# Kernel optimization log

Measured on AMD Instinct MI355X. Metric: run time of the kernel, lower is better.

The kernel has to match this reference:

```python
import jax, jax.numpy as jnp
import numpy as np

B, H, W, C = 2, 128, 128, 96
L = H * W
NUM_HEADS = 6
D_STATE = 16
DT_RANK = 6  # ceil(96/16)
D_CONV = 4
MLP_HIDDEN = 4 * C


def _layernorm(x, g, b, eps=1e-5):
    m = x.mean(-1, keepdims=True)
    v = x.var(-1, keepdims=True)
    return (x - m) * jax.lax.rsqrt(v + eps) * g + b


def _dwconv2d(x, w, b):
    # x: [B,C,H,W], w: [C,1,3,3] depthwise, padding=1 (torch 'same' for k=3)
    y = jax.lax.conv_general_dilated(x, w, (1, 1), [(1, 1), (1, 1)],
                                     dimension_numbers=('NCHW', 'OIHW', 'NCHW'),
                                     feature_group_count=x.shape[1])
    return y + b[None, :, None, None]


def _dwconv1d(x, w):
    # x: [B,C,L], w: [C,1,4]; torch padding='same' for even k=4 pads (1,2); bias is None (conv_bias//2 == 0)
    return jax.lax.conv_general_dilated(x, w, (1,), [(1, 2)],
                                        dimension_numbers=('NCH', 'OIH', 'NCH'),
                                        feature_group_count=x.shape[1])


def _rope(x):
    # x: [b, H, W, c]; 2D axial rotary embedding, k_max = c//4 per axis
    b, h, w, c = x.shape
    k_max = c // 4
    theta = 1.0 / (10000.0 ** (jnp.arange(k_max, dtype=jnp.float32) / k_max))
    ang_h = jnp.broadcast_to(jnp.arange(h, dtype=jnp.float32)[:, None, None] * theta, (h, w, k_max))
    ang_w = jnp.broadcast_to(jnp.arange(w, dtype=jnp.float32)[None, :, None] * theta, (h, w, k_max))
    angles = jnp.concatenate([ang_h, ang_w], -1)  # [h,w,c//2]
    cos, sin = jnp.cos(angles), jnp.sin(angles)
    xr, xi = x[..., 0::2], x[..., 1::2]  # consecutive pairs -> complex
    out_r = xr * cos - xi * sin
    out_i = xr * sin + xi * cos
    return jnp.stack([out_r, out_i], -1).reshape(x.shape)


def _linear_attention(x, qk_w, qk_b, lepe_w, lepe_b):
    # x: [b, n, c]
    b, n, c = x.shape
    hd = c // NUM_HEADS
    qk = x @ qk_w + qk_b  # [b,n,2c]
    q = jax.nn.elu(qk[..., :c]) + 1.0
    k = jax.nn.elu(qk[..., c:]) + 1.0
    v = x
    q_r = _rope(q.reshape(b, H, W, c)).reshape(b, n, NUM_HEADS, hd).transpose(0, 2, 1, 3)
    k_r = _rope(k.reshape(b, H, W, c)).reshape(b, n, NUM_HEADS, hd).transpose(0, 2, 1, 3)
    qh = q.reshape(b, n, NUM_HEADS, hd).transpose(0, 2, 1, 3)
    kh = k.reshape(b, n, NUM_HEADS, hd).transpose(0, 2, 1, 3)
    vh = v.reshape(b, n, NUM_HEADS, hd).transpose(0, 2, 1, 3)
    kmean = kh.mean(axis=2, keepdims=True)  # [b,h,1,hd]
    zden = 1.0 / (jnp.einsum('bhnd,bhmd->bhnm', qh, kmean) + 1e-6)  # [b,h,n,1]
    scale = n ** (-0.5)
    kv = jnp.einsum('bhnd,bhne->bhde', k_r * scale, vh * scale)  # [b,h,hd,hd]
    out = jnp.einsum('bhnd,bhde->bhne', q_r, kv) * zden
    out = out.transpose(0, 2, 1, 3).reshape(b, n, c)
    v2d = v.reshape(b, H, W, c).transpose(0, 3, 1, 2)
    lepe = _dwconv2d(v2d, lepe_w, lepe_b).transpose(0, 2, 3, 1).reshape(b, n, c)
    return out + lepe


def _selective_scan(u, delta, A, Bm, Cm, Dv):
    # u, delta: [b,d,l]; A: [d,n]; Bm, Cm: [b,n,l]; Dv: [d]
    dA = jnp.exp(jnp.einsum('bdl,dn->lbdn', delta, A))
    dBu = jnp.einsum('bdl,bnl,bdl->lbdn', delta, Bm, u)
    Ct = jnp.moveaxis(Cm, -1, 0)  # [l,b,n]

    def step(hcar, inp):
        dA_t, dBu_t, C_t = inp
        hcar = dA_t * hcar + dBu_t  # [b,d,n]
        y_t = jnp.einsum('bdn,bn->bd', hcar, C_t)
        return hcar, y_t

    h0 = jnp.zeros(dA.shape[1:], dtype=u.dtype)
    _, ys = jax.lax.scan(step, h0, (dA, dBu, Ct))  # ys: [l,b,d]
    y = jnp.moveaxis(ys, 0, -1)  # [b,d,l]
    return y + Dv[None, :, None] * u


def setup_inputs() -> dict:
    key = jax.random.key(0)
    ks = iter(jax.random.split(key, 40))

    def rn(shape, s=0.02):
        return jax.random.normal(next(ks), shape, jnp.float32) * s

    dt = jnp.exp(jax.random.uniform(next(ks), (C,), jnp.float32)
                 * (np.log(0.1) - np.log(0.001)) + np.log(0.001))
    dt_proj_b = dt + jnp.log(-jnp.expm1(-dt))
    return {
        'hidden_states': jax.random.normal(next(ks), (B, L, C), jnp.float32),
        'norm_in_g': jnp.ones((C,), jnp.float32),
        'norm_in_b': jnp.zeros((C,), jnp.float32),
        'in_proj_w': rn((C, 3 * C)),
        'dw_w': rn((C, 1, 3, 3)),
        'dw_b': rn((C,)),
        'qk_w': rn((C, 2 * C)),
        'qk_b': rn((2 * C,)),
        'lepe_w': rn((C, 1, 3, 3)),
        'lepe_b': rn((C,)),
        'conv_x_w': rn((C, 1, D_CONV)),
        'conv_z_w': rn((C, 1, D_CONV)),
        'x_proj_w': rn((C, DT_RANK + 2 * D_STATE)),
        'dt_proj_w': rn((DT_RANK, C), DT_RANK ** -0.5),
        'dt_proj_b': dt_proj_b,
        'A_log': jnp.log(jnp.broadcast_to(jnp.arange(1, D_STATE + 1, dtype=jnp.float32), (C, D_STATE)) + 0.0),
        'D': jnp.ones((C,), jnp.float32),
        'out_proj_w': rn((2 * C, C)),
        'proj_out_w': rn((C, C)),
        'proj_out_b': rn((C,)),
        'out_w': rn((2 * C, C)),
        'out_b': rn((C,)),
        'norm_mlp_g': jnp.ones((C,), jnp.float32),
        'norm_mlp_b': jnp.zeros((C,), jnp.float32),
        'fc1_w': rn((C, MLP_HIDDEN)),
        'fc1_b': rn((MLP_HIDDEN,)),
        'fc2_w': rn((MLP_HIDDEN, C)),
        'fc2_b': rn((C,)),
    }


def reference(hidden_states, norm_in_g, norm_in_b, in_proj_w, dw_w, dw_b, qk_w, qk_b,
              lepe_w, lepe_b, conv_x_w, conv_z_w, x_proj_w, dt_proj_w, dt_proj_b,
              A_log, D, out_proj_w, proj_out_w, proj_out_b, out_w, out_b,
              norm_mlp_g, norm_mlp_b, fc1_w, fc1_b, fc2_w, fc2_b):
    b, l, c = hidden_states.shape
    shortcut = hidden_states
    hs = _layernorm(hidden_states, norm_in_g, norm_in_b)
    xzw = jnp.transpose(hs @ in_proj_w, (0, 2, 1))  # [b,3c,l]
    x, z, w_ = jnp.split(xzw, 3, axis=1)  # each [b,c,l]
    # linear-attention branch
    lin_x = jax.nn.silu(_dwconv2d(w_.reshape(b, c, H, W), dw_w, dw_b))
    lin_x = jnp.transpose(lin_x, (0, 2, 3, 1)).reshape(b, l, c)
    lin_x = _linear_attention(lin_x, qk_w, qk_b, lepe_w, lepe_b)
    # selective-scan branch
    A = -jnp.exp(A_log)
    x = jax.nn.silu(_dwconv1d(x, conv_x_w))
    z = jax.nn.silu(_dwconv1d(z, conv_z_w))
    x_dbl = jnp.einsum('bdl,de->ble', x, x_proj_w)
    dt = x_dbl[..., :DT_RANK]
    Bm = jnp.transpose(x_dbl[..., DT_RANK:DT_RANK + D_STATE], (0, 2, 1))
    Cm = jnp.transpose(x_dbl[..., DT_RANK + D_STATE:], (0, 2, 1))
    delta = jax.nn.softplus(jnp.einsum('blr,rd->bdl', dt, dt_proj_w) + dt_proj_b[None, :, None])
    y = _selective_scan(x, delta, A, Bm, Cm, D)
    y = jnp.concatenate([y, z], axis=1)  # [b,2c,l]
    out1 = jnp.transpose(y, (0, 2, 1)) @ out_proj_w  # [b,l,c]
    z_t = jnp.transpose(z, (0, 2, 1))
    out2 = (lin_x * z_t) @ proj_out_w + proj_out_b
    out = jnp.concatenate([out1, out2], -1) @ out_w + out_b
    out = shortcut + out
    h2 = _layernorm(out, norm_mlp_g, norm_mlp_b)
    h2 = jax.nn.gelu(h2 @ fc1_w + fc1_b, approximate=False)
    return out + (h2 @ fc2_w + fc2_b)
```

## Files before the change

### kernel.cpp

```cpp
#include <hip/hip_runtime.h>
#include <hip/hip_bf16.h>
#include <hip/hip_fp16.h>
#include <math.h>

#define B_ 2
#define H_ 128
#define W_ 128
#define C_ 96
#define L_ (H_*W_)
#define BL_ (B_*L_)
#define NH_ 6
#define NPROJ_ 38
#define MLPH_ 384
#define NCH_ 512
#define CHL_ (L_/NCH_)
#define NG_ 32

typedef __attribute__((ext_vector_type(8))) short bf16x8;
typedef __attribute__((ext_vector_type(4))) float f32x4;
typedef __attribute__((ext_vector_type(4))) unsigned short us4v;

#define MFMA16(a,b,c) __builtin_amdgcn_mfma_f32_16x16x32_bf16(a,b,c,0,0,0)

#define WOFF1 0
#define WOFF2 54
#define WOFF3 90
#define WOFF4 126
#define WOFF5 144
#define WOFF6 180
#define WOFF7 252
#define WOFF8 324
#define WFRAGS 333

__device__ __forceinline__ float siluf(float x){ return x / (1.f + __expf(-x)); }
__device__ __forceinline__ unsigned short f2bf(float x){
    __hip_bfloat16 h = __float2bfloat16(x);
    return *reinterpret_cast<unsigned short*>(&h);
}
__device__ __forceinline__ unsigned pack2(float a, float b){
    return (unsigned)f2bf(a) | ((unsigned)f2bf(b) << 16);
}
__device__ __forceinline__ float bf2f(unsigned short u){
    return __uint_as_float((unsigned)u << 16);
}
__device__ __forceinline__ unsigned short f2h(float x){
    __half h = __float2half(x);
    return *reinterpret_cast<unsigned short*>(&h);
}
__device__ __forceinline__ float h2f(unsigned short u){
    __half h = *reinterpret_cast<__half*>(&u);
    return __half2float(h);
}
__device__ __forceinline__ float gelu_fast(float x){
    float u_ = 0.7978845608f*x*(1.f + 0.044715f*x*x);
    float au = fabsf(u_);
    float e = __expf(-2.f*au);
    float th = (1.f - e)/(1.f + e);
    th = copysignf(th, u_);
    return 0.5f*x*(1.f + th);
}

__global__ __launch_bounds__(64) void k_setup(const float* __restrict__ w1,
    const float* __restrict__ w2, const float* __restrict__ w3,
    const float* __restrict__ w4, const float* __restrict__ w5,
    const float* __restrict__ w6, const float* __restrict__ w7,
    const float* __restrict__ dww, const float* __restrict__ lw,
    const float* __restrict__ xpw, const float* __restrict__ cxw,
    const float* __restrict__ czw,
    unsigned short* __restrict__ dst, float2* __restrict__ ctab,
    float* __restrict__ wt9, float* __restrict__ lw9, float* __restrict__ kvacc,
    float* __restrict__ wxT, float* __restrict__ wzT)
{
    int m = blockIdx.y;
    int l = threadIdx.x;
    if (m < 7){
        const float* srcs[7] = {w1,w2,w3,w4,w5,w6,w7};
        const int Ks[7]   = {96,96,192,96,192,96,384};
        const int Ns[7]   = {288,192,96,96,96,384,96};
        const int offs[7] = {WOFF1,WOFF2,WOFF3,WOFF4,WOFF5,WOFF6,WOFF7};
        int f = blockIdx.x;
        int nnt = Ns[m] >> 4, nkf = Ks[m] >> 5;
        if (f >= nnt*nkf) return;
        int kf = f / nnt, nt = f - kf*nnt;
        const float* s = srcs[m];
        unsigned short* d = dst + ((size_t)(offs[m] + f)*64 + l)*8;
        int krow = kf*32 + (l>>4)*8;
        int col  = nt*16 + (l&15);
        #pragma unroll
        for (int j=0;j<8;j++) d[j] = f2bf(s[(size_t)(krow+j)*Ns[m] + col]);
    } else {
        int x = blockIdx.x;
        if (x == 0){
            for (int i=l; i<128*24; i+=64){
                int pos = i/24, p = i%24;
                float th = powf(10000.f, -(float)p/24.f);
                float sn, cs; sincosf((float)pos*th, &sn, &cs);
                ctab[i] = make_float2(cs, sn);
            }
        } else if (x == 1){
            for (int i=l; i<3264; i+=64) kvacc[i] = 0.f;
        } else if (x == 2){
            for (int i=l; i<864; i+=64){
                int c = i/9, tap = i%9;
                wt9[tap*96 + c] = dww[i];
                lw9[tap*96 + c] = lw[i];
            }
        } else if (x == 3){
            for (int f=0; f<9; f++){
                int kf=f/3, nt=f%3;
                unsigned short* d = dst + ((size_t)(WOFF8 + f)*64 + l)*8;
                int krow = kf*32 + (l>>4)*8;
                int col  = nt*16 + (l&15);
                #pragma unroll
                for (int j=0;j<8;j++){
                    float v = (col < NPROJ_) ? xpw[(size_t)(krow+j)*NPROJ_ + col] : 0.f;
                    d[j] = f2bf(v);
                }
            }
        } else if (x == 4){
            for (int i=l; i<384; i+=64){
                int j = i/96, c = i%96;
                wxT[i] = cxw[c*4 + j];
                wzT[i] = czw[c*4 + j];
            }
        }
    }
}

__global__ __launch_bounds__(256) void k_ln_inproj_m(const float* __restrict__ hs,
    const float* __restrict__ gg, const float* __restrict__ bb,
    const unsigned short* __restrict__ wbf,
    unsigned short* __restrict__ xx, unsigned short* __restrict__ zz,
    unsigned short* __restrict__ ww, unsigned short* __restrict__ hsb)
{
    __shared__ unsigned short A[64*128];
    int t = threadIdx.x;
    size_t row0 = (size_t)blockIdx.x * 64;
    {
        int r = t >> 2, q = t & 3;
        const float* src = hs + (row0 + r)*C_ + q*24;
        float v[24];
        float s=0.f, s2=0.f;
        #pragma unroll
        for (int i=0;i<24;i++){ float x=src[i]; v[i]=x; s+=x; s2+=x*x; }
        unsigned short* hdst = hsb + (row0 + r)*C_ + q*24;
        #pragma unroll
        for (int i=0;i<24;i+=4){
            us4v hv; hv[0]=f2bf(v[i]); hv[1]=f2bf(v[i+1]);
            hv[2]=f2bf(v[i+2]); hv[3]=f2bf(v[i+3]);
            *(us4v*)&hdst[i] = hv;
        }
        s += __shfl_xor(s,1); s2 += __shfl_xor(s2,1);
        s += __shfl_xor(s,2); s2 += __shfl_xor(s2,2);
        float mn = s*(1.f/C_);
        float rs = rsqrtf(s2*(1.f/C_) - mn*mn + 1e-5f);
        int base = r*128, sw = (r&7)<<3;
        #pragma unroll
        for (int i=0;i<24;i+=2){
            int c = q*24 + i;
            float a0 = (v[i]  -mn)*rs*gg[c]   + bb[c];
            float a1 = (v[i+1]-mn)*rs*gg[c+1] + bb[c+1];
            *(unsigned*)&A[base + (c ^ sw)] = pack2(a0,a1);
        }
    }
    __syncthreads();
    int w = t>>6, l = t&63, lr = l&15, lh = l>>4;
    int arow = w*16 + lr;
    int abase = arow*128, asw = (arow&7)<<3;
    bf16x8 af[3];
    #pragma unroll
    for (int kf=0;kf<3;kf++)
        af[kf] = *(const bf16x8*)&A[abase + ((kf*32 + lh*8) ^ asw)];
    #pragma unroll 2
    for (int nt=0; nt<18; nt++){
        f32x4 acc = {0.f,0.f,0.f,0.f};
        #pragma unroll
        for (int kf=0;kf<3;kf++){
            bf16x8 bf_ = *(const bf16x8*)(wbf + ((size_t)((WOFF1 + kf*18 + nt)*64 + l))*8);
            acc = MFMA16(af[kf], bf_, acc);
        }
        unsigned short* base_;
        if (nt < 6) base_ = xx; else if (nt < 12) base_ = zz; else base_ = ww;
        int col = (nt%6)*16 + lr;
        unsigned short* dst = base_ + (row0 + w*16 + lh*4)*C_ + col;
        #pragma unroll
        for (int j=0;j<4;j++) dst[(size_t)j*C_] = f2bf(acc[j]);
    }
}

__global__ __launch_bounds__(384) void k_conv1d_xdbl(const unsigned short* __restrict__ xxb,
    const unsigned short* __restrict__ zzb, const float* __restrict__ wxT,
    const float* __restrict__ wzT, const unsigned short* __restrict__ wbf,
    const float* __restrict__ dtw, const float* __restrict__ dtb,
    const float* __restrict__ A_log,
    unsigned short* __restrict__ xsb, unsigned short* __restrict__ zb,
    unsigned short* __restrict__ dlh, float* __restrict__ BC,
    float* __restrict__ Ap, float* __restrict__ Be)
{
    __shared__ unsigned short A[64*128];
    __shared__ float XD[64][8];
    __shared__ float dtws[6][96];
    __shared__ float sdl[64][96];
    __shared__ float sbc[64][32];
    int t = threadIdx.x;
    size_t row0 = (size_t)blockIdx.x * 64;
    int b = (int)(row0 >> 14);
    int l0 = (int)(row0 & 16383);
    for (int i=t; i<576; i+=384) dtws[i/96][i%96] = dtw[i];
    for (int p=t; p<64*24; p+=384){
        int r = p/24, cq = p - r*24, c = cq*4;
        int l = l0 + r;
        float ax0=0.f,ax1=0.f,ax2=0.f,ax3=0.f;
        float az0=0.f,az1=0.f,az2=0.f,az3=0.f;
        #pragma unroll
        for (int j=0;j<4;j++){
            int lq = l - 1 + j;
            if ((unsigned)lq < (unsigned)L_){
                size_t off = ((size_t)(b<<14) + lq)*C_ + c;
                us4v xv = *(const us4v*)&xxb[off];
                us4v zv = *(const us4v*)&zzb[off];
                float4 wx4 = *(const float4*)&wxT[j*96 + c];
                float4 wz4 = *(const float4*)&wzT[j*96 + c];
                ax0 += bf2f(xv[0])*wx4.x; ax1 += bf2f(xv[1])*wx4.y;
                ax2 += bf2f(xv[2])*wx4.z; ax3 += bf2f(xv[3])*wx4.w;
                az0 += bf2f(zv[0])*wz4.x; az1 += bf2f(zv[1])*wz4.y;
                az2 += bf2f(zv[2])*wz4.z; az3 += bf2f(zv[3])*wz4.w;
            }
        }
        ax0=siluf(ax0); ax1=siluf(ax1); ax2=siluf(ax2); ax3=siluf(ax3);
        az0=siluf(az0); az1=siluf(az1); az2=siluf(az2); az3=siluf(az3);
        us4v xo; xo[0]=f2bf(ax0); xo[1]=f2bf(ax1); xo[2]=f2bf(ax2); xo[3]=f2bf(ax3);
        *(us4v*)&xsb[(row0+r)*C_ + c] = xo;
        us4v zo; zo[0]=f2bf(az0); zo[1]=f2bf(az1); zo[2]=f2bf(az2); zo[3]=f2bf(az3);
        *(us4v*)&zb[(row0+r)*C_ + c] = zo;
        int sw = (r&7)<<3;
        *(us4v*)&A[r*128 + (c ^ sw)] = xo;
    }
    __syncthreads();
    int w=t>>6, l=t&63, lr=l&15, lh=l>>4;
    if (w < 4){
        int arow = w*16+lr, asw=(arow&7)<<3;
        bf16x8 af[3];
        #pragma unroll
        for (int kf=0;kf<3;kf++)
            af[kf] = *(const bf16x8*)&A[arow*128 + ((kf*32 + lh*8) ^ asw)];
        #pragma unroll
        for (int nt=0; nt<3; nt++){
            f32x4 acc={0.f,0.f,0.f,0.f};
            #pragma unroll
            for (int kf=0;kf<3;kf++){
                bf16x8 bfr=*(const bf16x8*)(wbf + ((size_t)((WOFF8 + kf*3 + nt)*64 + l))*8);
                acc = MFMA16(af[kf], bfr, acc);
            }
            int col = nt*16 + lr;
            #pragma unroll
            for (int j=0;j<4;j++){
                int row = w*16 + lh*4 + j;
                if (col < 6) XD[row][col] = acc[j];
                else if (col < NPROJ_){
                    BC[(row0+row)*32 + (col-6)] = acc[j];
                    sbc[row][col-6] = acc[j];
                }
            }
        }
    }
    __syncthreads();
    if (t < 256){
        int r = t>>2, q = t&3;
        float xd0=XD[r][0], xd1=XD[r][1], xd2=XD[r][2];
        float xd3=XD[r][3], xd4=XD[r][4], xd5=XD[r][5];
        #pragma unroll
        for (int g=0; g<6; g++){
            int c = q*24 + g*4;
            float4 acc = *(const float4*)&dtb[c];
            float4 w0 = *(const float4*)&dtws[0][c];
            float4 w1 = *(const float4*)&dtws[1][c];
            float4 w2 = *(const float4*)&dtws[2][c];
            float4 w3 = *(const float4*)&dtws[3][c];
            float4 w4 = *(const float4*)&dtws[4][c];
            float4 w5 = *(const float4*)&dtws[5][c];
            acc.x += xd0*w0.x + xd1*w1.x + xd2*w2.x + xd3*w3.x + xd4*w4.x + xd5*w5.x;
            acc.y += xd0*w0.y + xd1*w1.y + xd2*w2.y + xd3*w3.y + xd4*w4.y + xd5*w5.y;
            acc.z += xd0*w0.z + xd1*w1.z + xd2*w2.z + xd3*w3.z + xd4*w4.z + xd5*w5.z;
            acc.w += xd0*w0.w + xd1*w1.w + xd2*w2.w + xd3*w3.w + xd4*w4.w + xd5*w5.w;
            float4 dl;
            dl.x = (acc.x>20.f)? acc.x : __logf(1.f+__expf(acc.x));
            dl.y = (acc.y>20.f)? acc.y : __logf(1.f+__expf(acc.y));
            dl.z = (acc.z>20.f)? acc.z : __logf(1.f+__expf(acc.z));
            dl.w = (acc.w>20.f)? acc.w : __logf(1.f+__expf(acc.w));
            sdl[r][c]=dl.x; sdl[r][c+1]=dl.y; sdl[r][c+2]=dl.z; sdl[r][c+3]=dl.w;
            us4v dh; dh[0]=f2h(dl.x); dh[1]=f2h(dl.y); dh[2]=f2h(dl.z); dh[3]=f2h(dl.w);
            *(us4v*)&dlh[(row0+r)*C_ + c] = dh;
        }
    }
    __syncthreads();
    {
        int c = t>>2, nq = t&3;
        float4 a4 = *(const float4*)&A_log[c*16 + nq*4];
        float a0=-__expf(a4.x), a1=-__expf(a4.y), a2=-__expf(a4.z), a3=-__expf(a4.w);
        int chbase = b*NCH_ + (l0>>5);
        int csw_c = c;
        #pragma unroll
        for (int chunk=0; chunk<2; chunk++){
            float ap0=1.f,ap1=1.f,ap2=1.f,ap3=1.f;
            float be0=0.f,be1=0.f,be2=0.f,be3=0.f;
            for (int i=0;i<CHL_;i++){
                int row = chunk*CHL_ + i;
                float dl = sdl[row][c];
                float u = bf2f(A[row*128 + (csw_c ^ ((row&7)<<3))]);
                float du = dl*u;
                float4 bc = *(const float4*)&sbc[row][nq*4];
                float e0=__expf(dl*a0), e1=__expf(dl*a1), e2=__expf(dl*a2), e3=__expf(dl*a3);
                ap0*=e0; be0=be0*e0+du*bc.x;
                ap1*=e1; be1=be1*e1+du*bc.y;
                ap2*=e2; be2=be2*e2+du*bc.z;
                ap3*=e3; be3=be3*e3+du*bc.w;
            }
            size_t o = (size_t)(chbase+chunk)*1536 + c*16 + nq*4;
            float4 apv={ap0,ap1,ap2,ap3}, bev={be0,be1,be2,be3};
            *(float4*)&Ap[o] = apv;
            *(float4*)&Be[o] = bev;
        }
    }
}

__global__ __launch_bounds__(256) void k_qk_kv(const unsigned short* __restrict__ wwb,
    const float* __restrict__ wt9, const float* __restrict__ dwb,
    const unsigned short* __restrict__ wbf, const float* __restrict__ qkb,
    const float2* __restrict__ ctab, unsigned short* __restrict__ linb,
    unsigned short* __restrict__ qo, float* __restrict__ kvacc)
{
    __shared__ unsigned short A[64*128];
    __shared__ float KR[64*105];
    __shared__ float kmsum[96];
    int t = threadIdx.x;
    size_t row0 = (size_t)blockIdx.x * 64;
    int b = (int)(row0 >> 14);
    int l0 = (int)(row0 & 16383);
    for (int p = t; p < 64*24; p += 256){
        int r = p/24, cq = p - r*24, c = cq*4;
        int ll = l0 + r;
        int hq = ll>>7, wq = ll&127;
        float a0=0.f,a1=0.f,a2=0.f,a3=0.f;
        #pragma unroll
        for (int kh=0; kh<3; kh++){
            int hh = hq + kh - 1;
            if ((unsigned)hh < 128u){
                int base_row = (b<<14) + (hh<<7);
                #pragma unroll
                for (int kw=0; kw<3; kw++){
                    int wp = wq + kw - 1;
                    if ((unsigned)wp < 128u){
                        us4v v = *(const us4v*)&wwb[(size_t)(base_row + wp)*C_ + c];
                        float4 wt = *(const float4*)&wt9[(kh*3+kw)*96 + c];
                        a0 += bf2f(v[0])*wt.x; a1 += bf2f(v[1])*wt.y;
                        a2 += bf2f(v[2])*wt.z; a3 += bf2f(v[3])*wt.w;
                    }
                }
            }
        }
        float4 bv = *(const float4*)&dwb[c];
        us4v o;
        o[0]=f2bf(siluf(a0+bv.x)); o[1]=f2bf(siluf(a1+bv.y));
        o[2]=f2bf(siluf(a2+bv.z)); o[3]=f2bf(siluf(a3+bv.w));
        *(us4v*)&linb[(row0+r)*C_ + c] = o;
        int sw = (r&7)<<3;
        *(us4v*)&A[r*128 + (c ^ sw)] = o;
    }
    if (t < 96) kmsum[t] = 0.f;
    __syncthreads();
    int w=t>>6, l=t&63, lr=l&15, lh=l>>4;
    int arow = w*16+lr; int asw=(arow&7)<<3;
    bf16x8 af[3];
    #pragma unroll
    for (int kf=0;kf<3;kf++)
        af[kf] = *(const bf16x8*)&A[arow*128 + ((kf*32 + lh*8) ^ asw)];
    #pragma unroll 2
    for (int nt=0; nt<12; nt++){
        f32x4 acc={0.f,0.f,0.f,0.f};
        #pragma unroll
        for (int kf=0;kf<3;kf++){
            bf16x8 bfr=*(const bf16x8*)(wbf + ((size_t)((WOFF2 + kf*12 + nt)*64 + l))*8);
            acc = MFMA16(af[kf], bfr, acc);
        }
        int colg = nt*16 + lr;
        float bias = qkb[colg];
        float vv[4];
        #pragma unroll
        for (int j=0;j<4;j++){
            float v = acc[j] + bias;
            vv[j] = (v>0.f)? v+1.f : __expf(v);
        }
        if (nt < 6){
            unsigned short* dp = qo + (row0 + w*16 + lh*4)*C_ + colg;
            #pragma unroll
            for (int j=0;j<4;j++) dp[(size_t)j*C_] = f2bf(vv[j]);
        } else {
            int ck = colg - 96;
            atomicAdd(&kmsum[ck], vv[0]+vv[1]+vv[2]+vv[3]);
            float pv[4];
            #pragma unroll
            for (int j=0;j<4;j++) pv[j] = __shfl_xor(vv[j], 1);
            int p = ck >> 1;
            #pragma unroll
            for (int j=0;j<4;j++){
                int rl = l0 + w*16 + lh*4 + j;
                int hp = rl>>7, wp = rl&127;
                float2 cssn = (p<24)? ctab[hp*24+p] : ctab[wp*24+(p-24)];
                float kr = (ck&1)? (pv[j]*cssn.y + vv[j]*cssn.x)
                                 : (vv[j]*cssn.x - pv[j]*cssn.y);
                KR[(w*16+lh*4+j)*105 + ck] = kr;
            }
        }
    }
    __syncthreads();
    for (int h = w; h < 6; h += 4){
        f32x4 acc = {0.f,0.f,0.f,0.f};
        #pragma unroll
        for (int kk=0; kk<2; kk++){
            union { bf16x8 v; unsigned short u[8]; } afu, bfu;
            #pragma unroll
            for (int j=0;j<8;j++){
                int rr = kk*32 + lh*8 + j;
                afu.u[j] = f2bf(KR[rr*105 + h*16 + lr]);
                bfu.u[j] = A[rr*128 + ((h*16+lr) ^ ((rr&7)<<3))];
            }
            acc = MFMA16(afu.v, bfu.v, acc);
        }
        #pragma unroll
        for (int i=0;i<4;i++)
            atomicAdd(&kvacc[b*1536 + h*256 + (lh*4+i)*16 + lr], acc[i]);
    }
    if (t < 96) atomicAdd(&kvacc[3072 + b*96 + t], kmsum[t]);
}

__global__ __launch_bounds__(384) void k_attnout(const unsigned short* __restrict__ qb,
    const unsigned short* __restrict__ vb, const unsigned short* __restrict__ zb,
    const float* __restrict__ kvacc, const float2* __restrict__ ctab,
    const float* __restrict__ lw9, const float* __restrict__ lb,
    unsigned short* __restrict__ azb)
{
    __shared__ float kvs[1536];
    __shared__ float kms[96];
    int t = threadIdx.x;
    size_t row0 = (size_t)blockIdx.x * 16;
    int b = (int)(row0 >> 14);
    const float invL = 1.f/16384.f;
    for (int i=t; i<1536; i+=384) kvs[i] = kvacc[b*1536+i]*invL;
    if (t < 96) kms[t] = kvacc[3072+b*96+t]*invL;
    __syncthreads();
    int r = t/24, c4 = t%24;
    int c = c4*4;
    int lrow = (int)(row0 & 16383) + r;
    int hp = lrow>>7, wp = lrow&127;
    size_t row = row0 + r;
    us4v qu = *(const us4v*)&qb[row*C_ + c];
    float q0=bf2f(qu[0]), q1=bf2f(qu[1]), q2=bf2f(qu[2]), q3=bf2f(qu[3]);
    int p0 = c>>1, p1 = p0+1;
    float2 cs0 = (p0<24)? ctab[hp*24+p0] : ctab[wp*24+(p0-24)];
    float2 cs1 = (p1<24)? ctab[hp*24+p1] : ctab[wp*24+(p1-24)];
    float4 qr;
    qr.x = q0*cs0.x - q1*cs0.y;
    qr.y = q0*cs0.y + q1*cs0.x;
    qr.z = q2*cs1.x - q3*cs1.y;
    qr.w = q2*cs1.y + q3*cs1.x;
    int h = c4>>2, j = c4&3;
    int dbase = j*4;
    float zp = q0*kms[h*16+dbase]   + q1*kms[h*16+dbase+1]
             + q2*kms[h*16+dbase+2] + q3*kms[h*16+dbase+3];
    zp += __shfl_xor(zp,1);
    zp += __shfl_xor(zp,2);
    float zd = 1.f/(zp + 1e-6f);
    float4 o = {0.f,0.f,0.f,0.f};
    #pragma unroll
    for (int g=0; g<4; g++){
        float4 qg;
        if (g==0) qg = qr;
        else {
            qg.x=__shfl_xor(qr.x,g); qg.y=__shfl_xor(qr.y,g);
            qg.z=__shfl_xor(qr.z,g); qg.w=__shfl_xor(qr.w,g);
        }
        int db = ((j^g)<<2);
        const float* kp = &kvs[h*256 + db*16 + j*4];
        #pragma unroll
        for (int i=0;i<4;i++){
            float qi = (i==0)?qg.x:(i==1)?qg.y:(i==2)?qg.z:qg.w;
            float4 kv4 = *(const float4*)&kp[i*16];
            o.x += qi*kv4.x; o.y += qi*kv4.y;
            o.z += qi*kv4.z; o.w += qi*kv4.w;
        }
    }
    float4 acc = *(const float4*)&lb[c];
    #pragma unroll
    for (int kh=0; kh<3; kh++){
        int hh = hp + kh - 1;
        if ((unsigned)hh < 128u){
            int base_row = (b<<14) + (hh<<7);
            #pragma unroll
            for (int kw=0; kw<3; kw++){
                int wq = wp + kw - 1;
                if ((unsigned)wq < 128u){
                    us4v v = *(const us4v*)&vb[(size_t)(base_row + wq)*C_ + c];
                    float4 wt = *(const float4*)&lw9[(kh*3+kw)*96 + c];
                    acc.x += bf2f(v[0])*wt.x; acc.y += bf2f(v[1])*wt.y;
                    acc.z += bf2f(v[2])*wt.z; acc.w += bf2f(v[3])*wt.w;
                }
            }
        }
    }
    us4v zu = *(const us4v*)&zb[row*C_ + c];
    us4v res;
    res[0] = f2bf((o.x*zd + acc.x)*bf2f(zu[0]));
    res[1] = f2bf((o.y*zd + acc.y)*bf2f(zu[1]));
    res[2] = f2bf((o.z*zd + acc.z)*bf2f(zu[2]));
    res[3] = f2bf((o.w*zd + acc.w)*bf2f(zu[3]));
    *(us4v*)&azb[row*C_ + c] = res;
}

__global__ __launch_bounds__(384) void k_scan2a(const float* __restrict__ Ap,
    const float* __restrict__ Be, float* __restrict__ GA, float* __restrict__ GB)
{
    int t = threadIdx.x; int blk = blockIdx.x;
    int b = blk>>5, g = blk&(NG_-1);
    int idx = (t>>2)*16 + (t&3)*4;
    float4 A = {1.f,1.f,1.f,1.f}, Bv = {0.f,0.f,0.f,0.f};
    for (int j=0;j<16;j++){
        size_t o = ((size_t)(b*NCH_ + g*16 + j))*1536 + idx;
        float4 a = *(const float4*)&Ap[o];
        float4 bb = *(const float4*)&Be[o];
        Bv.x=a.x*Bv.x+bb.x; Bv.y=a.y*Bv.y+bb.y; Bv.z=a.z*Bv.z+bb.z; Bv.w=a.w*Bv.w+bb.w;
        A.x*=a.x; A.y*=a.y; A.z*=a.z; A.w*=a.w;
    }
    size_t o = (size_t)blk*1536 + idx;
    *(float4*)&GA[o] = A;
    *(float4*)&GB[o] = Bv;
}

__global__ __launch_bounds__(384) void k_scan2bc(const float* __restrict__ Ap,
    const float* __restrict__ Be, const float* __restrict__ GA,
    const float* __restrict__ GB, float* __restrict__ Hin)
{
    int t = threadIdx.x; int blk = blockIdx.x;
    int b = blk>>5, g = blk&(NG_-1);
    int idx = (t>>2)*16 + (t&3)*4;
    float4 h = {0.f,0.f,0.f,0.f};
    for (int gg=0; gg<g; gg++){
        size_t o = ((size_t)(b*NG_+gg))*1536 + idx;
        float4 a = *(const float4*)&GA[o];
        float4 bb = *(const float4*)&GB[o];
        h.x=a.x*h.x+bb.x; h.y=a.y*h.y+bb.y; h.z=a.z*h.z+bb.z; h.w=a.w*h.w+bb.w;
    }
    for (int j=0;j<16;j++){
        size_t o = ((size_t)(b*NCH_ + g*16 + j))*1536 + idx;
        *(float4*)&Hin[o] = h;
        float4 a = *(const float4*)&Ap[o];
        float4 bb = *(const float4*)&Be[o];
        h.x=a.x*h.x+bb.x; h.y=a.y*h.y+bb.y; h.z=a.z*h.z+bb.z; h.w=a.w*h.w+bb.w;
    }
}

__global__ __launch_bounds__(384) void k_scan3(const unsigned short* __restrict__ dlh,
    const unsigned short* __restrict__ xsb, const float* __restrict__ BC,
    const float* __restrict__ A_log, const float* __restrict__ Dv,
    const float* __restrict__ Hin, unsigned short* __restrict__ y)
{
    int t = threadIdx.x; int nq = t&3, c = t>>2;
    int blk = blockIdx.x; int b = blk>>9, ch = blk&(NCH_-1);
    float4 a4 = *(const float4*)&A_log[c*16 + nq*4];
    float a0=-__expf(a4.x), a1=-__expf(a4.y), a2=-__expf(a4.z), a3=-__expf(a4.w);
    float4 h = *(const float4*)&Hin[(size_t)blk*1536 + c*16 + nq*4];
    float Dc = Dv[c];
    size_t base = ((size_t)b<<14) + ch*CHL_;
    for (int i=0;i<CHL_;i++){
        size_t row = base + i;
        float dl = h2f(dlh[row*C_+c]);
        float u  = bf2f(xsb[row*C_+c]);
        float du = dl*u;
        float4 bcB = *(const float4*)&BC[row*32 + nq*4];
        float4 bcC = *(const float4*)&BC[row*32 + 16 + nq*4];
        float e0=__expf(dl*a0), e1=__expf(dl*a1), e2=__expf(dl*a2), e3=__expf(dl*a3);
        h.x=h.x*e0+du*bcB.x; h.y=h.y*e1+du*bcB.y;
        h.z=h.z*e2+du*bcB.z; h.w=h.w*e3+du*bcB.w;
        float yv = h.x*bcC.x + h.y*bcC.y + h.z*bcC.z + h.w*bcC.w;
        yv += __shfl_xor(yv,1);
        yv += __shfl_xor(yv,2);
        if (nq == 0) y[row*C_+c] = f2bf(yv + Dc*u);
    }
}

__global__ __launch_bounds__(512) void k_combine_mlp(const unsigned short* __restrict__ yb,
    const unsigned short* __restrict__ zb, const unsigned short* __restrict__ azb,
    const unsigned short* __restrict__ wbf, const float* __restrict__ pob,
    const float* __restrict__ outb, const unsigned short* __restrict__ hsb,
    const float* __restrict__ gg, const float* __restrict__ bb,
    const float* __restrict__ f1b, const float* __restrict__ f2b,
    float* __restrict__ outr)
{
    __shared__ __attribute__((aligned(16))) char POOL[65536];
    __shared__ float LNS[64][2], LNS2[64][2];
    unsigned short* C2 = (unsigned short*)POOL;
    unsigned short* AT = (unsigned short*)POOL;
    unsigned short* HID= (unsigned short*)(POOL + 16384);
    int t=threadIdx.x;
    size_t row0=(size_t)blockIdx.x*64;
    int w=t>>6, l=t&63, lr=l&15, lh=l>>4;
    int rt=w>>1, hf=w&1;
    int arow=rt*16+lr; int asw=(arow&7)<<3;
    size_t gbase = (row0+arow)*C_;
    bf16x8 af1[6], af2[3];
    #pragma unroll
    for (int kf=0;kf<3;kf++){
        af1[kf]   = *(const bf16x8*)&yb[gbase + kf*32 + lh*8];
        af1[3+kf] = *(const bf16x8*)&zb[gbase + kf*32 + lh*8];
        af2[kf]   = *(const bf16x8*)&azb[gbase + kf*32 + lh*8];
    }
    #pragma unroll
    for (int q=0;q<3;q++){
        int nt = hf*3 + q;
        f32x4 a1={0.f,0.f,0.f,0.f}, a2={0.f,0.f,0.f,0.f};
        #pragma unroll
        for (int kf=0;kf<6;kf++){
            bf16x8 b=*(const bf16x8*)(wbf+((size_t)((WOFF3+kf*6+nt)*64+l))*8);
            a1=MFMA16(af1[kf],b,a1);
        }
        #pragma unroll
        for (int kf=0;kf<3;kf++){
            bf16x8 b=*(const bf16x8*)(wbf+((size_t)((WOFF4+kf*6+nt)*64+l))*8);
            a2=MFMA16(af2[kf],b,a2);
        }
        int col=nt*16+lr;
        float pb=pob[col];
        #pragma unroll
        for (int j=0;j<4;j++){
            int row=rt*16+lh*4+j;
            int sw2=(row&7)<<3;
            C2[row*192 + (col^sw2)] = f2bf(a1[j]);
            C2[row*192 + ((96+col)^sw2)] = f2bf(a2[j]+pb);
        }
    }
    __syncthreads();
    bf16x8 af3[6];
    #pragma unroll
    for (int kf=0;kf<6;kf++) af3[kf]=*(const bf16x8*)&C2[arow*192 + ((kf*32+lh*8)^asw)];
    float outv[3][4];
    #pragma unroll
    for (int q=0;q<3;q++){
        int nt = hf*3 + q;
        f32x4 acc={0.f,0.f,0.f,0.f};
        #pragma unroll
        for (int kf=0;kf<6;kf++){
            bf16x8 b=*(const bf16x8*)(wbf+((size_t)((WOFF5+kf*6+nt)*64+l))*8);
            acc=MFMA16(af3[kf],b,acc);
        }
        int col=nt*16+lr;
        float ob=outb[col];
        #pragma unroll
        for (int j=0;j<4;j++){
            size_t row=row0+rt*16+lh*4+j;
            outv[q][j] = acc[j] + ob + bf2f(hsb[row*C_+col]);
        }
    }
    float s_[4], s2_[4];
    #pragma unroll
    for (int j=0;j<4;j++){
        float s=0.f, s2=0.f;
        #pragma unroll
        for (int q=0;q<3;q++){ float v=outv[q][j]; s+=v; s2+=v*v; }
        s_[j]=s; s2_[j]=s2;
    }
    #pragma unroll
    for (int m=1;m<16;m<<=1){
        #pragma unroll
        for (int j=0;j<4;j++){
            s_[j]  += __shfl_xor(s_[j],  m);
            s2_[j] += __shfl_xor(s2_[j], m);
        }
    }
    if (lr==0){
        #pragma unroll
        for (int j=0;j<4;j++){
            int row = rt*16+lh*4+j;
            LNS[row][hf]  = s_[j];
            LNS2[row][hf] = s2_[j];
        }
    }
    __syncthreads();
    #pragma unroll
    for (int j=0;j<4;j++){
        int row = rt*16+lh*4+j;
        float s  = LNS[row][0]  + LNS[row][1];
        float s2 = LNS2[row][0] + LNS2[row][1];
        float mn = s*(1.f/C_);
        float rs = rsqrtf(s2*(1.f/C_) - mn*mn + 1e-5f);
        int sw2 = (row&7)<<3;
        #pragma unroll
        for (int q=0;q<3;q++){
            int col = (hf*3+q)*16+lr;
            AT[row*128 + (col^sw2)] = f2bf((outv[q][j]-mn)*rs*gg[col]+bb[col]);
        }
    }
    __syncthreads();
    {
        bf16x8 af[3];
        #pragma unroll
        for(int kf=0;kf<3;kf++) af[kf]=*(const bf16x8*)&AT[arow*128+((kf*32+lh*8)^asw)];
        #pragma unroll 2
        for(int q=0;q<12;q++){
            int nt = hf*12 + q;
            f32x4 acc={0.f,0.f,0.f,0.f};
            #pragma unroll
            for(int kf=0;kf<3;kf++){
                bf16x8 b=*(const bf16x8*)(wbf+((size_t)((WOFF6+kf*24+nt)*64+l))*8);
                acc=MFMA16(af[kf],b,acc);
            }
            int col=nt*16+lr;
            float bias=f1b[col];
            #pragma unroll
            for(int j=0;j<4;j++){
                int row=rt*16+lh*4+j;
                HID[row*384 + (col^((row&7)<<3))] = f2bf(gelu_fast(acc[j]+bias));
            }
        }
    }
    __syncthreads();
    {
        bf16x8 afh[12];
        #pragma unroll
        for(int kf=0;kf<12;kf++) afh[kf]=*(const bf16x8*)&HID[arow*384+((kf*32+lh*8)^asw)];
        #pragma unroll
        for(int q=0;q<3;q++){
            int nt = hf*3 + q;
            f32x4 acc={0.f,0.f,0.f,0.f};
            #pragma unroll
            for(int kf=0;kf<12;kf++){
                bf16x8 b=*(const bf16x8*)(wbf+((size_t)((WOFF7+kf*6+nt)*64+l))*8);
                acc=MFMA16(afh[kf],b,acc);
            }
            int col=nt*16+lr;
            float bias=f2b[col];
            #pragma unroll
            for(int j=0;j<4;j++){
                size_t row=row0+rt*16+lh*4+j;
                outr[row*C_+col] = outv[q][j] + acc[j] + bias;
            }
        }
    }
}

extern "C" void kernel_launch(void* const* d_in, const int* in_sizes, int n_in,
                              void* d_out, int out_size, void* d_ws, size_t ws_size,
                              hipStream_t stream)
{
    const float* hs        = (const float*)d_in[0];
    const float* norm_in_g = (const float*)d_in[1];
    const float* norm_in_b = (const float*)d_in[2];
    const float* in_proj_w = (const float*)d_in[3];
    const float* dw_w      = (const float*)d_in[4];
    const float* dw_b      = (const float*)d_in[5];
    const float* qk_w      = (const float*)d_in[6];
    const float* qk_b      = (const float*)d_in[7];
    const float* lepe_w    = (const float*)d_in[8];
    const float* lepe_b    = (const float*)d_in[9];
    const float* conv_x_w  = (const float*)d_in[10];
    const float* conv_z_w  = (const float*)d_in[11];
    const float* x_proj_w  = (const float*)d_in[12];
    const float* dt_proj_w = (const float*)d_in[13];
    const float* dt_proj_b = (const float*)d_in[14];
    const float* A_log     = (const float*)d_in[15];
    const float* Dv        = (const float*)d_in[16];
    const float* out_proj_w= (const float*)d_in[17];
    const float* proj_out_w= (const float*)d_in[18];
    const float* proj_out_b= (const float*)d_in[19];
    const float* out_w     = (const float*)d_in[20];
    const float* out_b     = (const float*)d_in[21];
    const float* norm_mlp_g= (const float*)d_in[22];
    const float* norm_mlp_b= (const float*)d_in[23];
    const float* fc1_w     = (const float*)d_in[24];
    const float* fc1_b     = (const float*)d_in[25];
    const float* fc2_w     = (const float*)d_in[26];
    const float* fc2_b     = (const float*)d_in[27];

    float* ws = (float*)d_ws;
    size_t o = 0;
    const size_t USH = (size_t)BL_*C_/2;
    unsigned short* xxb  = (unsigned short*)(ws + o); o += USH;
    unsigned short* zzb  = (unsigned short*)(ws + o); o += USH;
    unsigned short* wwb  = (unsigned short*)(ws + o); o += USH;
    unsigned short* linb = (unsigned short*)(ws + o); o += USH;
    unsigned short* zbuf = (unsigned short*)(ws + o); o += USH;
    unsigned short* xsb  = (unsigned short*)(ws + o); o += USH;
    unsigned short* dlh  = (unsigned short*)(ws + o); o += USH;
    unsigned short* hsb  = (unsigned short*)(ws + o); o += USH;
    float* BC    = ws + o; o += (size_t)BL_*32;
    float* Ap    = ws + o; o += (size_t)B_*NCH_*1536;
    float* Be    = ws + o; o += (size_t)B_*NCH_*1536;
    float* Hin   = ws + o; o += (size_t)B_*NCH_*1536;
    float* GA    = ws + o; o += (size_t)B_*NG_*1536;
    float* GB    = ws + o; o += (size_t)B_*NG_*1536;
    float* kvacc = ws + o; o += 3264;
    float2* ctab = (float2*)(ws + o); o += 6144;
    float* wt9   = ws + o; o += 864;
    float* lw9   = ws + o; o += 864;
    float* wxT   = ws + o; o += 384;
    float* wzT   = ws + o; o += 384;
    unsigned short* wbf = (unsigned short*)(ws + o);

    unsigned short* qb  = xxb;
    unsigned short* yb  = zzb;
    unsigned short* azb = wwb;
    float* outr = (float*)d_out;

    k_setup<<<dim3(72,8), 64, 0, stream>>>(in_proj_w, qk_w, out_proj_w, proj_out_w,
                                           out_w, fc1_w, fc2_w, dw_w, lepe_w,
                                           x_proj_w, conv_x_w, conv_z_w,
                                           wbf, ctab, wt9, lw9, kvacc, wxT, wzT);
    k_ln_inproj_m<<<BL_/64, 256, 0, stream>>>(hs, norm_in_g, norm_in_b, wbf,
                                              xxb, zzb, wwb, hsb);
    k_conv1d_xdbl<<<BL_/64, 384, 0, stream>>>(xxb, zzb, wxT, wzT, wbf,
                                              dt_proj_w, dt_proj_b, A_log,
                                              xsb, zbuf, dlh, BC, Ap, Be);
    k_qk_kv<<<BL_/64, 256, 0, stream>>>(wwb, wt9, dw_b, wbf, qk_b, ctab,
                                        linb, qb, kvacc);
    k_attnout<<<BL_/16, 384, 0, stream>>>(qb, linb, zbuf, kvacc, ctab, lw9, lepe_b, azb);
    k_scan2a<<<B_*NG_, 384, 0, stream>>>(Ap, Be, GA, GB);
    k_scan2bc<<<B_*NG_, 384, 0, stream>>>(Ap, Be, GA, GB, Hin);
    k_scan3<<<B_*NCH_, 384, 0, stream>>>(dlh, xsb, BC, A_log, Dv, Hin, yb);
    k_combine_mlp<<<BL_/64, 512, 0, stream>>>(yb, zbuf, azb, wbf, proj_out_b,
                                              out_b, hsb, norm_mlp_g, norm_mlp_b,
                                              fc1_b, fc2_b, outr);
}
```

Before: 192.2 us.

## Split depthwise conv2d into own kernel and fold chunk-prefix scan into scan3

Moves the 3x3 depthwise conv + SiLU out of k_qk_kv into a standalone elementwise kernel, so k_qk_kv just loads the precomputed activations into shared memory. It also removes the k_scan2bc kernel and the Hin buffer: each k_scan3 block now recomputes its own starting state from the group prefixes (GA/GB) and the preceding chunk summaries within its group. This trades one launch and the Hin write/read for redundant per-block prefix work (up to 31+15 steps) and an extra kernel launch for the conv.

```diff
diff --git a/kernel.cpp b/kernel.cpp
--- a/kernel.cpp
+++ b/kernel.cpp
@@ -186,6 +186,40 @@
         #pragma unroll
         for (int j=0;j<4;j++) dst[(size_t)j*C_] = f2bf(acc[j]);
     }
+}
+
+__global__ __launch_bounds__(256) void k_dwconv2d(const unsigned short* __restrict__ wwb,
+    const float* __restrict__ wt9, const float* __restrict__ dwb,
+    unsigned short* __restrict__ out)
+{
+    int gid = blockIdx.x*256 + threadIdx.x;
+    int row = gid/24, c4 = gid%24; int c = c4*4;
+    int b = row >> 14;
+    int ll = row & (L_-1);
+    int h = ll >> 7, wq = ll & 127;
+    float a0=0.f,a1=0.f,a2=0.f,a3=0.f;
+    #pragma unroll
+    for (int kh=0; kh<3; kh++){
+        int hh = h + kh - 1;
+        if ((unsigned)hh < 128u){
+            int base_row = (b<<14) + (hh<<7);
+            #pragma unroll
+            for (int kw=0; kw<3; kw++){
+                int wp = wq + kw - 1;
+                if ((unsigned)wp < 128u){
+                    us4v v = *(const us4v*)&wwb[(size_t)(base_row + wp)*C_ + c];
+                    float4 wt = *(const float4*)&wt9[(kh*3+kw)*96 + c];
+                    a0 += bf2f(v[0])*wt.x; a1 += bf2f(v[1])*wt.y;
+                    a2 += bf2f(v[2])*wt.z; a3 += bf2f(v[3])*wt.w;
+                }
+            }
+        }
+    }
+    float4 bv = *(const float4*)&dwb[c];
+    us4v o;
+    o[0]=f2bf(siluf(a0+bv.x)); o[1]=f2bf(siluf(a1+bv.y));
+    o[2]=f2bf(siluf(a2+bv.z)); o[3]=f2bf(siluf(a3+bv.w));
+    *(us4v*)&out[(size_t)row*C_ + c] = o;
 }
 
 __global__ __launch_bounds__(384) void k_conv1d_xdbl(const unsigned short* __restrict__ xxb,
@@ -299,7 +333,6 @@
         float4 a4 = *(const float4*)&A_log[c*16 + nq*4];
         float a0=-__expf(a4.x), a1=-__expf(a4.y), a2=-__expf(a4.z), a3=-__expf(a4.w);
         int chbase = b*NCH_ + (l0>>5);
-        int csw_c = c;
         #pragma unroll
         for (int chunk=0; chunk<2; chunk++){
             float ap0=1.f,ap1=1.f,ap2=1.f,ap3=1.f;
@@ -307,7 +340,7 @@
             for (int i=0;i<CHL_;i++){
                 int row = chunk*CHL_ + i;
                 float dl = sdl[row][c];
-                float u = bf2f(A[row*128 + (csw_c ^ ((row&7)<<3))]);
+                float u = bf2f(A[row*128 + (c ^ ((row&7)<<3))]);
                 float du = dl*u;
                 float4 bc = *(const float4*)&sbc[row][nq*4];
                 float e0=__expf(dl*a0), e1=__expf(dl*a1), e2=__expf(dl*a2), e3=__expf(dl*a3);
@@ -324,11 +357,10 @@
     }
 }
 
-__global__ __launch_bounds__(256) void k_qk_kv(const unsigned short* __restrict__ wwb,
-    const float* __restrict__ wt9, const float* __restrict__ dwb,
+__global__ __launch_bounds__(256) void k_qk_kv(const unsigned short* __restrict__ lin,
     const unsigned short* __restrict__ wbf, const float* __restrict__ qkb,
-    const float2* __restrict__ ctab, unsigned short* __restrict__ linb,
-    unsigned short* __restrict__ qo, float* __restrict__ kvacc)
+    const float2* __restrict__ ctab, unsigned short* __restrict__ qo,
+    float* __restrict__ kvacc)
 {
     __shared__ unsigned short A[64*128];
     __shared__ float KR[64*105];
@@ -337,35 +369,10 @@
     size_t row0 = (size_t)blockIdx.x * 64;
     int b = (int)(row0 >> 14);
     int l0 = (int)(row0 & 16383);
-    for (int p = t; p < 64*24; p += 256){
-        int r = p/24, cq = p - r*24, c = cq*4;
-        int ll = l0 + r;
-        int hq = ll>>7, wq = ll&127;
-        float a0=0.f,a1=0.f,a2=0.f,a3=0.f;
-        #pragma unroll
-        for (int kh=0; kh<3; kh++){
-            int hh = hq + kh - 1;
-            if ((unsigned)hh < 128u){
-                int base_row = (b<<14) + (hh<<7);
-                #pragma unroll
-                for (int kw=0; kw<3; kw++){
-                    int wp = wq + kw - 1;
-                    if ((unsigned)wp < 128u){
-                        us4v v = *(const us4v*)&wwb[(size_t)(base_row + wp)*C_ + c];
-                        float4 wt = *(const float4*)&wt9[(kh*3+kw)*96 + c];
-                        a0 += bf2f(v[0])*wt.x; a1 += bf2f(v[1])*wt.y;
-                        a2 += bf2f(v[2])*wt.z; a3 += bf2f(v[3])*wt.w;
-                    }
-                }
-            }
-        }
-        float4 bv = *(const float4*)&dwb[c];
-        us4v o;
-        o[0]=f2bf(siluf(a0+bv.x)); o[1]=f2bf(siluf(a1+bv.y));
-        o[2]=f2bf(siluf(a2+bv.z)); o[3]=f2bf(siluf(a3+bv.w));
-        *(us4v*)&linb[(row0+r)*C_ + c] = o;
+    for (int p = t; p < 64*12; p += 256){
+        int r = p/12, c = (p - r*12)*8;
         int sw = (r&7)<<3;
-        *(us4v*)&A[r*128 + (c ^ sw)] = o;
+        *(uint4*)&A[r*128 + (c ^ sw)] = *(const uint4*)&lin[(row0+r)*C_ + c];
     }
     if (t < 96) kmsum[t] = 0.f;
     __syncthreads();
@@ -536,13 +543,19 @@
     *(float4*)&GB[o] = Bv;
 }
 
-__global__ __launch_bounds__(384) void k_scan2bc(const float* __restrict__ Ap,
-    const float* __restrict__ Be, const float* __restrict__ GA,
-    const float* __restrict__ GB, float* __restrict__ Hin)
-{
-    int t = threadIdx.x; int blk = blockIdx.x;
-    int b = blk>>5, g = blk&(NG_-1);
-    int idx = (t>>2)*16 + (t&3)*4;
+__global__ __launch_bounds__(384) void k_scan3(const unsigned short* __restrict__ dlh,
+    const unsigned short* __restrict__ xsb, const float* __restrict__ BC,
+    const float* __restrict__ A_log, const float* __restrict__ Dv,
+    const float* __restrict__ Ap, const float* __restrict__ Be,
+    const float* __restrict__ GA, const float* __restrict__ GB,
+    unsigned short* __restrict__ y)
+{
+    int t = threadIdx.x; int nq = t&3, c = t>>2;
+    int blk = blockIdx.x; int b = blk>>9, ch = blk&(NCH_-1);
+    int g = ch>>4, j0 = ch&15;
+    int idx = c*16 + nq*4;
+    float4 a4 = *(const float4*)&A_log[idx];
+    float a0=-__expf(a4.x), a1=-__expf(a4.y), a2=-__expf(a4.z), a3=-__expf(a4.w);
     float4 h = {0.f,0.f,0.f,0.f};
     for (int gg=0; gg<g; gg++){
         size_t o = ((size_t)(b*NG_+gg))*1536 + idx;
@@ -550,25 +563,12 @@
         float4 bb = *(const float4*)&GB[o];
         h.x=a.x*h.x+bb.x; h.y=a.y*h.y+bb.y; h.z=a.z*h.z+bb.z; h.w=a.w*h.w+bb.w;
     }
-    for (int j=0;j<16;j++){
-        size_t o = ((size_t)(b*NCH_ + g*16 + j))*1536 + idx;
-        *(float4*)&Hin[o] = h;
+    for (int jj=0; jj<j0; jj++){
+        size_t o = ((size_t)(b*NCH_ + g*16 + jj))*1536 + idx;
         float4 a = *(const float4*)&Ap[o];
         float4 bb = *(const float4*)&Be[o];
         h.x=a.x*h.x+bb.x; h.y=a.y*h.y+bb.y; h.z=a.z*h.z+bb.z; h.w=a.w*h.w+bb.w;
     }
-}
-
-__global__ __launch_bounds__(384) void k_scan3(const unsigned short* __restrict__ dlh,
-    const unsigned short* __restrict__ xsb, const float* __restrict__ BC,
-    const float* __restrict__ A_log, const float* __restrict__ Dv,
-    const float* __restrict__ Hin, unsigned short* __restrict__ y)
-{
-    int t = threadIdx.x; int nq = t&3, c = t>>2;
-    int blk = blockIdx.x; int b = blk>>9, ch = blk&(NCH_-1);
-    float4 a4 = *(const float4*)&A_log[c*16 + nq*4];
-    float a0=-__expf(a4.x), a1=-__expf(a4.y), a2=-__expf(a4.z), a3=-__expf(a4.w);
-    float4 h = *(const float4*)&Hin[(size_t)blk*1536 + c*16 + nq*4];
     float Dc = Dv[c];
     size_t base = ((size_t)b<<14) + ch*CHL_;
     for (int i=0;i<CHL_;i++){
@@ -794,7 +794,6 @@
     float* BC    = ws + o; o += (size_t)BL_*32;
     float* Ap    = ws + o; o += (size_t)B_*NCH_*1536;
     float* Be    = ws + o; o += (size_t)B_*NCH_*1536;
-    float* Hin   = ws + o; o += (size_t)B_*NCH_*1536;
     float* GA    = ws + o; o += (size_t)B_*NG_*1536;
     float* GB    = ws + o; o += (size_t)B_*NG_*1536;
     float* kvacc = ws + o; o += 3264;
@@ -816,15 +815,14 @@
                                            wbf, ctab, wt9, lw9, kvacc, wxT, wzT);
     k_ln_inproj_m<<<BL_/64, 256, 0, stream>>>(hs, norm_in_g, norm_in_b, wbf,
                                               xxb, zzb, wwb, hsb);
+    k_dwconv2d<<<(BL_*24)/256, 256, 0, stream>>>(wwb, wt9, dw_b, linb);
     k_conv1d_xdbl<<<BL_/64, 384, 0, stream>>>(xxb, zzb, wxT, wzT, wbf,
                                               dt_proj_w, dt_proj_b, A_log,
                                               xsb, zbuf, dlh, BC, Ap, Be);
-    k_qk_kv<<<BL_/64, 256, 0, stream>>>(wwb, wt9, dw_b, wbf, qk_b, ctab,
-                                        linb, qb, kvacc);
+    k_qk_kv<<<BL_/64, 256, 0, stream>>>(linb, wbf, qk_b, ctab, qb, kvacc);
     k_attnout<<<BL_/16, 384, 0, stream>>>(qb, linb, zbuf, kvacc, ctab, lw9, lepe_b, azb);
     k_scan2a<<<B_*NG_, 384, 0, stream>>>(Ap, Be, GA, GB);
-    k_scan2bc<<<B_*NG_, 384, 0, stream>>>(Ap, Be, GA, GB, Hin);
-    k_scan3<<<B_*NCH_, 384, 0, stream>>>(dlh, xsb, BC, A_log, Dv, Hin, yb);
+    k_scan3<<<B_*NCH_, 384, 0, stream>>>(dlh, xsb, BC, A_log, Dv, Ap, Be, GA, GB, yb);
     k_combine_mlp<<<BL_/64, 512, 0, stream>>>(yb, zbuf, azb, wbf, proj_out_b,
                                               out_b, hsb, norm_mlp_g, norm_mlp_b,
                                               fc1_b, fc2_b, outr);
```

Result: no change. 194.1 us (+1.0%).
